# Optimization experiments

Hardware: AMD Instinct MI355X
Metric: run time of the kernel (lower is better)

The kernel has to match this reference:

```python
import jax, jax.numpy as jnp
import numpy as np


def conv2d(x, w, bias, stride=1, pad=0, groups=1):
    out = jax.lax.conv_general_dilated(
        x, w, (stride, stride), [(pad, pad), (pad, pad)],
        dimension_numbers=("NCHW", "OIHW", "NCHW"), feature_group_count=groups)
    return out + bias[None, :, None, None]


PATCHSIZE = [(4, 4), (8, 8)]
NEG = jnp.float32(-1e9)


def setup_inputs() -> dict:
    key = jax.random.key(0)
    ks = jax.random.split(key, 24)
    d = 128
    s = 0.05
    inp = {
        "x": jax.random.normal(ks[0], (16, d, 64, 64), jnp.float32),
        "m": jax.random.uniform(ks[1], (16, 1, 64, 64), jnp.float32),
        "depth_map": jax.random.normal(ks[2], (16, 1, 256, 256), jnp.float32),
        "wq": jax.random.normal(ks[3], (d, d, 1, 1), jnp.float32) * s,
        "bq": jax.random.normal(ks[4], (d,), jnp.float32) * s,
        "wk": jax.random.normal(ks[5], (d, d, 1, 1), jnp.float32) * s,
        "bk": jax.random.normal(ks[6], (d,), jnp.float32) * s,
        "wv": jax.random.normal(ks[7], (d, d, 1, 1), jnp.float32) * s,
        "bv": jax.random.normal(ks[8], (d,), jnp.float32) * s,
        "wvle": jax.random.normal(ks[9], (d, 1, 3, 3), jnp.float32) * s,  # depthwise
        "bvle": jax.random.normal(ks[10], (d,), jnp.float32) * s,
        "wd1": jax.random.normal(ks[11], (d, 1, 3, 3), jnp.float32) * s,
        "bd1": jax.random.normal(ks[12], (d,), jnp.float32) * s,
        "wd2": jax.random.normal(ks[13], (1, d, 3, 3), jnp.float32) * s,
        "bd2": jax.random.normal(ks[14], (1,), jnp.float32) * s,
        "wo": jax.random.normal(ks[15], (d, d, 3, 3), jnp.float32) * s,
        "bo": jax.random.normal(ks[16], (d,), jnp.float32) * s,
        "b": 2,
        "c": 128,
    }
    return inp


def _forward(x, m, depth_map, wq, bq, wk, bk, wv, bv, wvle, bvle,
             wd1, bd1, wd2, bd2, wo, bo, b, c):
    bt, _, h, w = x.shape
    t = bt // b
    d_k = c // len(PATCHSIZE)

    q_all = conv2d(x, wq, bq)
    k_all = conv2d(x, wk, bk)
    v_all = conv2d(x, wv, bv) + conv2d(x, wvle, bvle, pad=1, groups=c)
    d1 = jax.nn.relu(conv2d(depth_map, wd1, bd1, stride=2, pad=1))
    _depth = jax.nn.relu(conv2d(d1, wd2, bd2, stride=2, pad=1))  # (bt,1,h,w)

    outs = []
    for i, (width, height) in enumerate(PATCHSIZE):
        out_w, out_h = w // width, h // height
        L = t * out_h * out_w

        def patch(z, ch):
            # (b*t, ch, h, w) -> (b, L, ch*height*width)
            z = z.reshape(b, t, ch, out_h, height, out_w, width)
            return z.transpose(0, 1, 3, 5, 2, 4, 6).reshape(b, L, ch * height * width)

        mask = jnp.mean(patch(m, 1), -1) > 0.5            # (b, L) per-key mask
        dsort = jnp.sort(patch(_depth, 1), -1)            # (b, L, height*width)
        hw = height * width
        dmin, dmed, dmax = dsort[..., 0], dsort[..., (hw - 1) // 2], dsort[..., -1]

        q = patch(q_all[:, i * d_k:(i + 1) * d_k], d_k)
        k_ = patch(k_all[:, i * d_k:(i + 1) * d_k], d_k)
        v = patch(v_all[:, i * d_k:(i + 1) * d_k], d_k)

        scale = 1.0 / jnp.sqrt(jnp.float32(q.shape[-1]))
        s = jnp.einsum("bqd,bkd->bqk", q, k_) * scale     # shared QK^T

        def head(dbias):
            ss = s * jax.nn.sigmoid(dbias)[:, None, :]
            ss = jnp.where(mask[:, None, :], NEG, ss)
            return jnp.einsum("bqk,bkd->bqd", jax.nn.softmax(ss, -1), v)

        y = (head(dmed) + head(dmax) + head(dmin)) / 3.0
        y = y.reshape(b, t, out_h, out_w, d_k, height, width)
        y = y.transpose(0, 1, 4, 2, 5, 3, 6).reshape(bt, d_k, h, w)
        outs.append(y)

    out = jnp.concatenate(outs, 1)
    out = conv2d(out, wo, bo, pad=1)
    out = jnp.where(out >= 0, out, 0.2 * out)  # LeakyReLU(0.2)
    return out


def reference(x, m, depth_map, wq, bq, wk, bk, wv, bv, wvle, bvle,
              wd1, bd1, wd2, bd2, wo, bo, b, c):
    out = _forward(x, m, depth_map, wq, bq, wk, bk, wv, bv, wvle, bvle,
                   wd1, bd1, wd2, bd2, wo, bo, b, c)
    return (out, depth_map)
```

## Files before the change

kernel.cpp:

```cpp
#include <hip/hip_runtime.h>
#include <cmath>

typedef unsigned short u16;
typedef __attribute__((ext_vector_type(8))) __bf16 bf16x8;
typedef __attribute__((ext_vector_type(4))) float f32x4;

constexpr int Bb = 2, Tt = 8, Dc = 128, PIX = 4096;

__device__ inline u16 f2bf(float f) {
    unsigned u = __builtin_bit_cast(unsigned, f);
    u += 0x7fffu + ((u >> 16) & 1u);
    return (u16)(u >> 16);
}
__device__ inline float bf2f(u16 h) {
    unsigned u = ((unsigned)h) << 16;
    return __builtin_bit_cast(float, u);
}

#define GLOAD16(gp, lp) __builtin_amdgcn_global_load_lds( \
    (const __attribute__((address_space(1))) void*)(const void*)(gp), \
    (__attribute__((address_space(3))) void*)(void*)(lp), 16, 0, 0)

__device__ inline void mfma_chunk(const u16* lAs, const u16* lBs, int wave, int lane,
                                  f32x4 (&acc)[4][4])
{
    const int wm = (wave >> 1) * 64, wn = (wave & 1) * 64;
    const int fr = lane & 15;
    const int q4 = lane >> 4;
    const int sw = (q4 ^ ((fr >> 1) & 3)) * 8;
    bf16x8 av[4], bv[4];
#pragma unroll
    for (int i = 0; i < 4; ++i) av[i] = *(const bf16x8*)&lAs[(wm + i * 16 + fr) * 32 + sw];
#pragma unroll
    for (int j = 0; j < 4; ++j) bv[j] = *(const bf16x8*)&lBs[(wn + j * 16 + fr) * 32 + sw];
#pragma unroll
    for (int i = 0; i < 4; ++i)
#pragma unroll
        for (int j = 0; j < 4; ++j)
            acc[i][j] = __builtin_amdgcn_mfma_f32_16x16x32_bf16(av[i], bv[j], acc[i][j], 0, 0, 0);
}

__device__ inline void mfma_nt(const u16* A, int ldkA, const u16* B, int ldkB,
                               int kChunks, int wave, int lane,
                               u16* lAs, u16* lBs, f32x4 (&acc)[4][4])
{
    const int r = lane >> 2;
    const int kq8 = ((lane & 3) ^ ((r >> 1) & 3)) * 8;
    const u16* ga0 = A + (size_t)(wave * 32 + r) * ldkA + kq8;
    const u16* ga1 = ga0 + (size_t)16 * ldkA;
    const u16* gb0 = B + (size_t)(wave * 32 + r) * ldkB + kq8;
    const u16* gb1 = gb0 + (size_t)16 * ldkB;
    for (int kb = 0; kb < kChunks; kb += 2) {
        __syncthreads();
        GLOAD16(ga0 + kb * 32, lAs + wave * 1024);
        GLOAD16(ga1 + kb * 32, lAs + wave * 1024 + 512);
        GLOAD16(gb0 + kb * 32, lBs + wave * 1024);
        GLOAD16(gb1 + kb * 32, lBs + wave * 1024 + 512);
        GLOAD16(ga0 + (kb + 1) * 32, lAs + 4096 + wave * 1024);
        GLOAD16(ga1 + (kb + 1) * 32, lAs + 4096 + wave * 1024 + 512);
        GLOAD16(gb0 + (kb + 1) * 32, lBs + 4096 + wave * 1024);
        GLOAD16(gb1 + (kb + 1) * 32, lBs + 4096 + wave * 1024 + 512);
        __syncthreads();
        mfma_chunk(lAs, lBs, wave, lane, acc);
        mfma_chunk(lAs + 4096, lBs + 4096, wave, lane, acc);
    }
}

__global__ void k_prep(const float* __restrict__ wq, const float* __restrict__ wk,
                       const float* __restrict__ wv, const float* __restrict__ wo,
                       u16* __restrict__ Wqkv, u16* __restrict__ WoT)
{
    int idx = blockIdx.x * 256 + threadIdx.x;
    if (idx < 49152) {
        const float* w = idx < 16384 ? wq : (idx < 32768 ? wk : wv);
        Wqkv[idx] = f2bf(w[idx & 16383]);
    }
    int j = idx - 49152;
    if (j >= 0 && j < 147456) {
        int tap = j / 16384, rem = j % 16384;
        WoT[j] = f2bf(wo[(size_t)rem * 9 + tap]);
    }
}

__global__ __launch_bounds__(256) void k_xt(const float* __restrict__ x, u16* __restrict__ Xt)
{
    __shared__ float ls[128 * 65];
    const int n = blockIdx.y, pix0 = blockIdx.x * 64;
#pragma unroll
    for (int rep = 0; rep < 32; ++rep) {
        int idx = rep * 256 + threadIdx.x;
        int cin = idx >> 6, p = idx & 63;
        ls[cin * 65 + p] = x[((size_t)n * Dc + cin) * PIX + pix0 + p];
    }
    __syncthreads();
#pragma unroll
    for (int rep = 0; rep < 32; ++rep) {
        int idx = rep * 256 + threadIdx.x;
        int p = idx >> 7, cin = idx & 127;
        Xt[((size_t)n * PIX + pix0 + p) * Dc + cin] = f2bf(ls[cin * 65 + p]);
    }
}

__global__ __launch_bounds__(256) void k_qkv_mfma(const u16* __restrict__ Wqkv,
                                                  const u16* __restrict__ Xt,
                                                  const float* __restrict__ bq,
                                                  const float* __restrict__ bk,
                                                  const float* __restrict__ bv,
                                                  u16* __restrict__ Qp0, u16* __restrict__ Kp0,
                                                  u16* __restrict__ Qp1, u16* __restrict__ Kp1,
                                                  u16* __restrict__ v_bf)
{
    __shared__ u16 lAs[8192], lBs[8192];
    const int tid = threadIdx.x, wave = tid >> 6, lane = tid & 63;
    const int mt = blockIdx.y, n = blockIdx.z, px0 = blockIdx.x * 128;
    f32x4 acc[4][4];
#pragma unroll
    for (int i = 0; i < 4; ++i)
#pragma unroll
        for (int j = 0; j < 4; ++j) acc[i][j] = (f32x4){0.f, 0.f, 0.f, 0.f};
    mfma_nt(Wqkv + (size_t)mt * 128 * 128, 128,
            Xt + ((size_t)n * PIX + px0) * 128, 128, 4, wave, lane, lAs, lBs, acc);
    const int wm = (wave >> 1) * 64, wn = (wave & 1) * 64;
    const int rb = (lane >> 4) * 4, cb = lane & 15;
    const int bi = n >> 3, ti = n & 7;
    if (mt < 2) {
        const float* bp = (mt == 0) ? bq : bk;
        u16* d0 = (mt == 0) ? Qp0 : Kp0;
        u16* d1 = (mt == 0) ? Qp1 : Kp1;
#pragma unroll
        for (int i = 0; i < 4; ++i)
#pragma unroll
            for (int reg = 0; reg < 4; ++reg) {
                int c = wm + i * 16 + rb + reg;
                float bias = bp[c];
#pragma unroll
                for (int j = 0; j < 4; ++j) {
                    int pix = px0 + wn + j * 16 + cb;
                    int y = pix >> 6, x = pix & 63;
                    u16 val = f2bf(acc[i][j][reg] + bias);
                    if (c < 64) {
                        int l = ti * 256 + (y >> 2) * 16 + (x >> 2);
                        int f = c * 16 + (y & 3) * 4 + (x & 3);
                        d0[((size_t)bi * 2048 + l) * 1024 + f] = val;
                    } else {
                        int l = ti * 64 + (y >> 3) * 8 + (x >> 3);
                        int f = (c - 64) * 64 + (y & 7) * 8 + (x & 7);
                        d1[((size_t)bi * 512 + l) * 4096 + f] = val;
                    }
                }
            }
    } else {
#pragma unroll
        for (int i = 0; i < 4; ++i)
#pragma unroll
            for (int reg = 0; reg < 4; ++reg) {
                int c = wm + i * 16 + rb + reg;
                float bias = bv[c];
#pragma unroll
                for (int j = 0; j < 4; ++j) {
                    int pix = px0 + wn + j * 16 + cb;
                    v_bf[((size_t)n * Dc + c) * PIX + pix] = f2bf(acc[i][j][reg] + bias);
                }
            }
    }
}

__global__ __launch_bounds__(256) void k_vdw(const float* __restrict__ X,
                                             const float* __restrict__ wvle,
                                             const float* __restrict__ bvle,
                                             u16* __restrict__ v_bf)
{
    __shared__ float ls[4096];
    const int c = blockIdx.x, n = blockIdx.y;
    const int tid = threadIdx.x;
    const float* xp = X + ((size_t)n * Dc + c) * PIX;
#pragma unroll
    for (int r = 0; r < 4; ++r)
        *(float4*)&ls[r * 1024 + tid * 4] = *(const float4*)&xp[r * 1024 + tid * 4];
    __syncthreads();
    float w[9];
#pragma unroll
    for (int t = 0; t < 9; ++t) w[t] = wvle[c * 9 + t];
    const float bias = bvle[c];
    const int x = tid & 63, y0 = (tid >> 6) * 16;
    const bool xl = (x > 0), xr = (x < 63);
    u16* vp = v_bf + ((size_t)n * Dc + c) * PIX;
#pragma unroll
    for (int r = 0; r < 16; ++r) {
        int y = y0 + r;
        float s = bias;
#pragma unroll
        for (int ky = 0; ky < 3; ++ky) {
            int yy = y + ky - 1;
            if (yy < 0 || yy > 63) continue;
            const float* row = &ls[yy * 64];
            float m  = row[x];
            float lv = xl ? row[x - 1] : 0.f;
            float rv = xr ? row[x + 1] : 0.f;
            s += w[ky * 3 + 0] * lv + w[ky * 3 + 1] * m + w[ky * 3 + 2] * rv;
        }
        int idx = y * 64 + x;
        vp[idx] = f2bf(bf2f(vp[idx]) + s);
    }
}

__global__ __launch_bounds__(256) void k_d1(const float* __restrict__ dm,
                                            const float* __restrict__ wd1,
                                            const float* __restrict__ bd1,
                                            u16* __restrict__ d1b)
{
    __shared__ float ls[17 * 132];
    const int n = blockIdx.y;
    const int yt = blockIdx.x >> 1, xh = blockIdx.x & 1;
    const int Y0 = yt * 8;
    const int tid = threadIdx.x;
    const float* dmp = dm + (size_t)n * 65536;
    for (int idx = tid; idx < 17 * 132; idx += 256) {
        int row = idx / 132, cl = idx % 132;
        int gr = 2 * Y0 - 1 + row;
        int gc = 128 * xh - 1 + cl;
        float v = 0.f;
        if (gr >= 0 && gr < 256 && gc >= 0 && gc < 256 && cl < 129) v = dmp[gr * 256 + gc];
        ls[idx] = v;
    }
    __syncthreads();
    const int Xl = tid & 63;
    const int Yl0 = tid >> 6;
    float in0[9], in1[9];
#pragma unroll
    for (int jy = 0; jy < 3; ++jy)
#pragma unroll
        for (int jx = 0; jx < 3; ++jx) {
            in0[jy * 3 + jx] = ls[(2 * Yl0 + jy) * 132 + 2 * Xl + jx];
            in1[jy * 3 + jx] = ls[(2 * (Yl0 + 4) + jy) * 132 + 2 * Xl + jx];
        }
    const int X = 64 * xh + Xl;
    u16* outbase = d1b + (size_t)n * Dc * 16384 + (size_t)Y0 * 128 + X;
    for (int c = 0; c < 128; ++c) {
        const float* w1 = wd1 + c * 9;
        float a0 = bd1[c], a1 = a0;
#pragma unroll
        for (int t = 0; t < 9; ++t) { a0 += w1[t] * in0[t]; a1 += w1[t] * in1[t]; }
        u16* ob = outbase + (size_t)c * 16384;
        ob[(size_t)Yl0 * 128]       = f2bf(fmaxf(a0, 0.f));
        ob[(size_t)(Yl0 + 4) * 128] = f2bf(fmaxf(a1, 0.f));
    }
}

__global__ __launch_bounds__(256) void k_d2p(const u16* __restrict__ d1b,
                                             const float* __restrict__ wd2,
                                             float* __restrict__ part)
{
    __shared__ u16 ls[33 * 136];
    const int yt = blockIdx.x, n = blockIdx.y, cg = blockIdx.z;
    const int tid = threadIdx.x;
    const int y0 = yt * 16;
    if (tid < 33) ls[tid * 136 + 7] = 0;
    const int x = tid & 63;
    const int yl0 = (tid >> 6) * 4;
    float acc[4] = {0.f, 0.f, 0.f, 0.f};
    for (int c = 0; c < 16; ++c) {
        const u16* src = d1b + ((size_t)n * Dc + cg * 16 + c) * 16384;
        __syncthreads();
        for (int idx = tid; idx < 33 * 16; idx += 256) {
            int row = idx >> 4, s = idx & 15;
            int gr = 2 * y0 - 1 + row;
            uint4 v = make_uint4(0, 0, 0, 0);
            if (gr >= 0 && gr < 128) v = *(const uint4*)(src + gr * 128 + s * 8);
            *(uint4*)&ls[row * 136 + 8 + s * 8] = v;
        }
        __syncthreads();
        const float* w2 = wd2 + (cg * 16 + c) * 9;
        float w[9];
#pragma unroll
        for (int t = 0; t < 9; ++t) w[t] = w2[t];
#pragma unroll
        for (int r = 0; r < 4; ++r) {
            int yl = yl0 + r;
#pragma unroll
            for (int ky = 0; ky < 3; ++ky) {
                const u16* rp = &ls[(2 * yl + ky) * 136 + 2 * x + 7];
                float v0 = bf2f(rp[0]);
                unsigned pr = *(const unsigned*)(rp + 1);
                float v1 = bf2f((u16)(pr & 0xffffu));
                float v2 = bf2f((u16)(pr >> 16));
                acc[r] += w[ky * 3 + 0] * v0 + w[ky * 3 + 1] * v1 + w[ky * 3 + 2] * v2;
            }
        }
    }
    float* pp = part + ((size_t)cg * 16 + n) * PIX;
#pragma unroll
    for (int r = 0; r < 4; ++r)
        pp[(y0 + yl0 + r) * 64 + x] = acc[r];
}

__global__ void k_dfin(const float* __restrict__ part, const float* __restrict__ bd2,
                       float* __restrict__ dep)
{
    int idx = blockIdx.x * 256 + threadIdx.x;
    float s = bd2[0];
#pragma unroll
    for (int cg = 0; cg < 8; ++cg) s += part[(size_t)cg * 65536 + idx];
    dep[idx] = fmaxf(s, 0.f);
}

template<int PS>
__global__ __launch_bounds__(256) void k_stats2(const float* __restrict__ mI,
                                                const float* __restrict__ dep,
                                                float* __restrict__ maskf,
                                                float* __restrict__ smed,
                                                float* __restrict__ smaxA,
                                                float* __restrict__ sminA,
                                                int outn, int L)
{
    constexpr int HW = PS * PS;
    constexpr int TPB = 256 / HW;
    const int tok = blockIdx.x * TPB + threadIdx.x / HW;
    const int el  = threadIdx.x % HW;
    if (tok >= Bb * L) return;
    const int bi = tok / L, l = tok % L;
    const int ti = l / (outn * outn); const int rem = l % (outn * outn);
    const int oh = rem / outn, ow = rem % outn;
    const int n = bi * Tt + ti;
    const int py = el / PS, px = el % PS;
    const size_t off = (size_t)n * PIX + (size_t)(oh * PS + py) * 64 + ow * PS + px;
    const float mv = mI[off];
    const float dv = dep[off];
    float msum = mv, vmin = dv, vmax = dv;
#pragma unroll
    for (int o = HW / 2; o > 0; o >>= 1) {
        msum += __shfl_xor(msum, o);
        vmin = fminf(vmin, __shfl_xor(vmin, o));
        vmax = fmaxf(vmax, __shfl_xor(vmax, o));
    }
    const int gbase = (threadIdx.x & 63) & ~(HW - 1);
    int cl = 0, ce = 0;
#pragma unroll
    for (int b2 = 0; b2 < HW; ++b2) {
        float vb = __shfl(dv, gbase + b2);
        cl += (vb < dv);
        ce += (vb == dv);
    }
    constexpr int kk = (HW - 1) / 2;
    if (el == 0) {
        maskf[tok] = (msum / (float)HW > 0.5f) ? 1.f : 0.f;
        smaxA[tok] = 1.f / (1.f + __expf(-vmax));
        sminA[tok] = 1.f / (1.f + __expf(-vmin));
    }
    if (cl <= kk && kk < cl + ce)
        smed[tok] = 1.f / (1.f + __expf(-dv));
}

__global__ void k_patchT(const u16* __restrict__ v_bf, u16* __restrict__ Vt,
                         int ps, int outn, int L, int F, int cbase)
{
    size_t idx = (size_t)blockIdx.x * 256 + threadIdx.x;
    size_t total = (size_t)Bb * F * L / 4;
    if (idx >= total) return;
    int l0 = (int)((idx * 4) % L);
    size_t t2 = (idx * 4) / L;
    int f = (int)(t2 % F);
    int bi = (int)(t2 / F);
    int hw = ps * ps;
    int c = cbase + f / hw, r = f % hw;
    int py = r / ps, px = r % ps;
    int ti = l0 / (outn * outn); int rem = l0 % (outn * outn);
    int oh = rem / outn, ow0 = rem % outn;
    size_t base = ((size_t)(bi * Tt + ti) * Dc + c) * PIX + (oh * ps + py) * 64 + px;
    u16 out4[4];
#pragma unroll
    for (int e = 0; e < 4; ++e) out4[e] = v_bf[base + (size_t)(ow0 + e) * ps];
    *(uint2*)&Vt[((size_t)bi * F + f) * L + l0] = *(uint2*)out4;
}

__global__ __launch_bounds__(256) void k_qkT_mfma(const u16* __restrict__ Qp,
                                                  const u16* __restrict__ Kp,
                                                  u16* __restrict__ S,
                                                  int L, int F, int ksplit, float scale)
{
    __shared__ u16 lAs[8192], lBs[8192];
    const int tid = threadIdx.x, wave = tid >> 6, lane = tid & 63;
    const int bi = blockIdx.z / ksplit, ks = blockIdx.z % ksplit;
    const int kf = F / ksplit;
    f32x4 acc[4][4];
#pragma unroll
    for (int i = 0; i < 4; ++i)
#pragma unroll
        for (int j = 0; j < 4; ++j) acc[i][j] = (f32x4){0.f, 0.f, 0.f, 0.f};
    mfma_nt(Qp + (size_t)bi * L * F + (size_t)blockIdx.y * 128 * F + (size_t)ks * kf, F,
            Kp + (size_t)bi * L * F + (size_t)blockIdx.x * 128 * F + (size_t)ks * kf, F,
            kf / 32, wave, lane, lAs, lBs, acc);
    const int wm = (wave >> 1) * 64, wn = (wave & 1) * 64;
    const int rb = (lane >> 4) * 4, cb = lane & 15;
    u16* Cp = S + ((size_t)ks * Bb + bi) * L * L;
#pragma unroll
    for (int i = 0; i < 4; ++i)
#pragma unroll
        for (int reg = 0; reg < 4; ++reg) {
            int gm = blockIdx.y * 128 + wm + i * 16 + rb + reg;
#pragma unroll
            for (int j = 0; j < 4; ++j) {
                int gn = blockIdx.x * 128 + wn + j * 16 + cb;
                Cp[(size_t)gm * L + gn] = f2bf(acc[i][j][reg] * scale);
            }
        }
}

__device__ inline float blockMax(float v, float* sh) {
#pragma unroll
    for (int o = 32; o > 0; o >>= 1) v = fmaxf(v, __shfl_down(v, o));
    __syncthreads();
    if ((threadIdx.x & 63) == 0) sh[threadIdx.x >> 6] = v;
    __syncthreads();
    return fmaxf(fmaxf(sh[0], sh[1]), fmaxf(sh[2], sh[3]));
}
__device__ inline float blockSum(float v, float* sh) {
#pragma unroll
    for (int o = 32; o > 0; o >>= 1) v += __shfl_down(v, o);
    __syncthreads();
    if ((threadIdx.x & 63) == 0) sh[threadIdx.x >> 6] = v;
    __syncthreads();
    return sh[0] + sh[1] + sh[2] + sh[3];
}

template<int NPAIR, int NSPLIT>
__global__ __launch_bounds__(256) void k_softmax(const u16* __restrict__ S,
                                                 u16* __restrict__ Pb,
                                                 const float* __restrict__ maskf,
                                                 const float* __restrict__ smed,
                                                 const float* __restrict__ smaxA,
                                                 const float* __restrict__ sminA,
                                                 int L)
{
    __shared__ float sred[4];
    const int bi = blockIdx.y, q = blockIdx.x;
    const size_t pstr = (size_t)Bb * L * L;
    const u16* row = S + (size_t)bi * L * L + (size_t)q * L;
    u16* prow = Pb + (size_t)bi * L * L + (size_t)q * L;
    const float* mk  = maskf + bi * L;
    const float* s0p = smed  + bi * L;
    const float* s1p = smaxA + bi * L;
    const float* s2p = sminA + bi * L;
    const int tid = threadIdx.x;
    float a0[2 * NPAIR], a1[2 * NPAIR], a2[2 * NPAIR];
    float m0 = -3.4e38f, m1 = -3.4e38f, m2 = -3.4e38f;
#pragma unroll
    for (int e = 0; e < NPAIR; ++e) {
        int k = e * 512 + tid * 2;
        unsigned u = *(const unsigned*)&row[k];
        float sva = bf2f((u16)(u & 0xffffu));
        float svb = bf2f((u16)(u >> 16));
#pragma unroll
        for (int s2 = 1; s2 < NSPLIT; ++s2) {
            unsigned w = *(const unsigned*)&row[(size_t)s2 * pstr + k];
            sva += bf2f((u16)(w & 0xffffu));
            svb += bf2f((u16)(w >> 16));
        }
        float2 mv  = *(const float2*)&mk[k];
        float2 p0  = *(const float2*)&s0p[k];
        float2 p1  = *(const float2*)&s1p[k];
        float2 p2  = *(const float2*)&s2p[k];
        bool ma = mv.x > 0.5f, mb = mv.y > 0.5f;
        float v0a = ma ? -1e9f : sva * p0.x, v0b = mb ? -1e9f : svb * p0.y;
        float v1a = ma ? -1e9f : sva * p1.x, v1b = mb ? -1e9f : svb * p1.y;
        float v2a = ma ? -1e9f : sva * p2.x, v2b = mb ? -1e9f : svb * p2.y;
        a0[2 * e] = v0a; a0[2 * e + 1] = v0b;
        a1[2 * e] = v1a; a1[2 * e + 1] = v1b;
        a2[2 * e] = v2a; a2[2 * e + 1] = v2b;
        m0 = fmaxf(m0, fmaxf(v0a, v0b));
        m1 = fmaxf(m1, fmaxf(v1a, v1b));
        m2 = fmaxf(m2, fmaxf(v2a, v2b));
    }
    m0 = blockMax(m0, sred); m1 = blockMax(m1, sred); m2 = blockMax(m2, sred);
    float l0 = 0.f, l1 = 0.f, l2 = 0.f;
#pragma unroll
    for (int e = 0; e < 2 * NPAIR; ++e) {
        a0[e] = __expf(a0[e] - m0); l0 += a0[e];
        a1[e] = __expf(a1[e] - m1); l1 += a1[e];
        a2[e] = __expf(a2[e] - m2); l2 += a2[e];
    }
    l0 = blockSum(l0, sred); l1 = blockSum(l1, sred); l2 = blockSum(l2, sred);
    float c0 = 1.f / (3.f * l0), c1 = 1.f / (3.f * l1), c2 = 1.f / (3.f * l2);
#pragma unroll
    for (int e = 0; e < NPAIR; ++e) {
        int k = e * 512 + tid * 2;
        u16 oa = f2bf(a0[2 * e] * c0 + a1[2 * e] * c1 + a2[2 * e] * c2);
        u16 ob = f2bf(a0[2 * e + 1] * c0 + a1[2 * e + 1] * c1 + a2[2 * e + 1] * c2);
        unsigned pk = (unsigned)oa | ((unsigned)ob << 16);
        *(unsigned*)&prow[k] = pk;
    }
}

__global__ __launch_bounds__(256) void k_pv_mfma(const u16* __restrict__ Pb,
                                                 const u16* __restrict__ Vt,
                                                 u16* __restrict__ Yp,
                                                 int L, int F, int ksplit)
{
    __shared__ u16 lAs[8192], lBs[8192];
    const int tid = threadIdx.x, wave = tid >> 6, lane = tid & 63;
    const int bi = blockIdx.z / ksplit, ks = blockIdx.z % ksplit;
    const int kf = L / ksplit;
    f32x4 acc[4][4];
#pragma unroll
    for (int i = 0; i < 4; ++i)
#pragma unroll
        for (int j = 0; j < 4; ++j) acc[i][j] = (f32x4){0.f, 0.f, 0.f, 0.f};
    mfma_nt(Pb + (size_t)bi * L * L + (size_t)blockIdx.y * 128 * L + (size_t)ks * kf, L,
            Vt + (size_t)bi * F * L + (size_t)blockIdx.x * 128 * L + (size_t)ks * kf, L,
            kf / 32, wave, lane, lAs, lBs, acc);
    const int wm = (wave >> 1) * 64, wn = (wave & 1) * 64;
    const int rb = (lane >> 4) * 4, cb = lane & 15;
    u16* Cp = Yp + ((size_t)(ks * Bb + bi) * L) * F;
#pragma unroll
    for (int i = 0; i < 4; ++i)
#pragma unroll
        for (int reg = 0; reg < 4; ++reg) {
            int gm = blockIdx.y * 128 + wm + i * 16 + rb + reg;
#pragma unroll
            for (int j = 0; j < 4; ++j) {
                int gn = blockIdx.x * 128 + wn + j * 16 + cb;
                Cp[(size_t)gm * F + gn] = f2bf(acc[i][j][reg]);
            }
        }
}

template<int NSPLIT>
__global__ void k_unpatch(const u16* __restrict__ Yp, u16* __restrict__ catbT,
                          int ps, int outn, int L, int F, int cbase)
{
    size_t idx = (size_t)blockIdx.x * 256 + threadIdx.x;
    size_t total = (size_t)Bb * L * F / 4;
    if (idx >= total) return;
    const size_t pstr = (size_t)Bb * L * F;
    int f0 = (int)((idx * 4) % F);
    size_t t2 = (idx * 4) / F;
    int l = (int)(t2 % L);
    int bi = (int)(t2 / L);
    size_t off = ((size_t)bi * L + l) * F + f0;
    float s[4] = {0.f, 0.f, 0.f, 0.f};
#pragma unroll
    for (int sp = 0; sp < NSPLIT; ++sp) {
        uint2 u = *(const uint2*)&Yp[(size_t)sp * pstr + off];
        s[0] += bf2f((u16)(u.x & 0xffffu));
        s[1] += bf2f((u16)(u.x >> 16));
        s[2] += bf2f((u16)(u.y & 0xffffu));
        s[3] += bf2f((u16)(u.y >> 16));
    }
    int hw = ps * ps;
    int c = cbase + f0 / hw, r0 = f0 % hw;
    int ti = l / (outn * outn); int rem = l % (outn * outn);
    int oh = rem / outn, ow = rem % outn;
    int n = bi * Tt + ti;
    int py = r0 / ps, px = r0 % ps;
    size_t base = ((size_t)n * PIX + (size_t)(oh * ps + py) * 64 + ow * ps + px) * Dc + c;
#pragma unroll
    for (int e = 0; e < 4; ++e)
        catbT[base + (size_t)e * Dc] = f2bf(s[e]);
}

__global__ __launch_bounds__(256) void k_conv_mfma(const u16* __restrict__ catbT,
                                                   const u16* __restrict__ WoT,
                                                   const u16* __restrict__ zp,
                                                   u16* __restrict__ Cpart)
{
    __shared__ u16 lAs[8192], lBs[8192];
    const int tid = threadIdx.x, wave = tid >> 6, lane = tid & 63;
    const int pix0 = blockIdx.x * 128;
    const int sp = blockIdx.y;
    const int r = lane >> 2;
    const int kq8 = ((lane & 3) ^ ((r >> 1) & 3)) * 8;
    int yb[2], xb[2], nn[2];
#pragma unroll
    for (int s = 0; s < 2; ++s) {
        int pg = pix0 + wave * 32 + r + s * 16;
        nn[s] = pg >> 12; yb[s] = (pg >> 6) & 63; xb[s] = pg & 63;
    }
    const u16* gb_base = WoT + (size_t)(wave * 32 + r) * 128 + kq8;
    f32x4 acc[4][4];
#pragma unroll
    for (int i = 0; i < 4; ++i)
#pragma unroll
        for (int j = 0; j < 4; ++j) acc[i][j] = (f32x4){0.f, 0.f, 0.f, 0.f};
    for (int tp = 0; tp < 9; ++tp) {
        const int t0 = sp * 18 + tp * 2;
        __syncthreads();
#pragma unroll
        for (int h = 0; h < 2; ++h) {
            const int t = t0 + h;
            const int tap = t >> 2, kc = t & 3;
            const int dy = tap / 3 - 1, dx = tap % 3 - 1;
            const u16* ga[2];
#pragma unroll
            for (int s = 0; s < 2; ++s) {
                int y = yb[s] + dy, xx = xb[s] + dx;
                bool ok = ((unsigned)y < 64u) && ((unsigned)xx < 64u);
                ga[s] = ok ? catbT + (((size_t)(nn[s] << 12) + y * 64 + xx) << 7) + kq8 + kc * 32 : zp;
            }
            const u16* gb = gb_base + tap * 16384 + kc * 32;
            GLOAD16(ga[0], lAs + h * 4096 + wave * 1024);
            GLOAD16(ga[1], lAs + h * 4096 + wave * 1024 + 512);
            GLOAD16(gb, lBs + h * 4096 + wave * 1024);
            GLOAD16(gb + 2048, lBs + h * 4096 + wave * 1024 + 512);
        }
        __syncthreads();
        mfma_chunk(lAs, lBs, wave, lane, acc);
        mfma_chunk(lAs + 4096, lBs + 4096, wave, lane, acc);
    }
    const int wm = (wave >> 1) * 64, wn = (wave & 1) * 64;
    const int rb = (lane >> 4) * 4, cb = lane & 15;
    u16* Cp = Cpart + (size_t)sp * 8388608;
#pragma unroll
    for (int i = 0; i < 4; ++i)
#pragma unroll
        for (int reg = 0; reg < 4; ++reg) {
            int gm = pix0 + wm + i * 16 + rb + reg;
#pragma unroll
            for (int j = 0; j < 4; ++j) {
                int gn = wn + j * 16 + cb;
                Cp[(size_t)gm * 128 + gn] = f2bf(acc[i][j][reg]);
            }
        }
}

__global__ __launch_bounds__(256) void k_cfin(const u16* __restrict__ Cpart,
                                              const float* __restrict__ bo,
                                              float* __restrict__ outp)
{
    const int pg0 = blockIdx.x * 64;
    const int lane = threadIdx.x & 63, wv = threadIdx.x >> 6;
    const int pix = pg0 + lane;
    const int n = pix >> 12, p = pix & 4095;
    const u16* r0 = Cpart + (size_t)pix * 128 + wv * 32;
    const u16* r1 = r0 + 8388608;
#pragma unroll
    for (int c4 = 0; c4 < 8; ++c4) {
        uint2 a = *(const uint2*)(r0 + c4 * 4);
        uint2 b = *(const uint2*)(r1 + c4 * 4);
        float s[4];
        s[0] = bf2f((u16)(a.x & 0xffffu)) + bf2f((u16)(b.x & 0xffffu));
        s[1] = bf2f((u16)(a.x >> 16))     + bf2f((u16)(b.x >> 16));
        s[2] = bf2f((u16)(a.y & 0xffffu)) + bf2f((u16)(b.y & 0xffffu));
        s[3] = bf2f((u16)(a.y >> 16))     + bf2f((u16)(b.y >> 16));
#pragma unroll
        for (int e = 0; e < 4; ++e) {
            int cout = wv * 32 + c4 * 4 + e;
            float v = s[e] + bo[cout];
            v = (v >= 0.f) ? v : 0.2f * v;
            outp[((size_t)n * Dc + cout) * PIX + p] = v;
        }
    }
}

extern "C" void kernel_launch(void* const* d_in, const int* in_sizes, int n_in,
                              void* d_out, int out_size, void* d_ws, size_t ws_size,
                              hipStream_t stream)
{
    (void)in_sizes; (void)n_in; (void)out_size; (void)ws_size;
    const float* x    = (const float*)d_in[0];
    const float* mI   = (const float*)d_in[1];
    const float* dmap = (const float*)d_in[2];
    const float* wq   = (const float*)d_in[3];
    const float* bq   = (const float*)d_in[4];
    const float* wk   = (const float*)d_in[5];
    const float* bk   = (const float*)d_in[6];
    const float* wv   = (const float*)d_in[7];
    const float* bv   = (const float*)d_in[8];
    const float* wvle = (const float*)d_in[9];
    const float* bvle = (const float*)d_in[10];
    const float* wd1  = (const float*)d_in[11];
    const float* bd1  = (const float*)d_in[12];
    const float* wd2  = (const float*)d_in[13];
    const float* bd2  = (const float*)d_in[14];
    const float* wo   = (const float*)d_in[15];
    const float* bo   = (const float*)d_in[16];

    char* w8 = (char*)d_ws;
    u16*   v_bf  = (u16*)(w8);
    u16*   Xt    = (u16*)(w8 + 0x1000000);
    u16*   catbT = (u16*)(w8 + 0x2000000);
    u16*   Qp0   = (u16*)(w8 + 0x3000000);
    u16*   Kp0   = (u16*)(w8 + 0x3800000);
    u16*   Qp1   = (u16*)(w8 + 0x4000000);
    u16*   Kp1   = (u16*)(w8 + 0x4800000);
    u16*   Vt    = (u16*)(w8 + 0x5000000);
    u16*   Sb    = (u16*)(w8 + 0x5800000);
    u16*   Pb    = (u16*)(w8 + 0x7800000);
    u16*   Yp    = (u16*)(w8 + 0x8800000);
    u16*   Cpart = (u16*)(w8 + 0x5800000);
    u16*   d1b   = (u16*)(w8 + 0x3000000);
    float* dep   = (float*)(w8 + 0xA800000);
    float* maskf = (float*)(w8 + 0xA840000);
    float* smed  = (float*)(w8 + 0xA844000);
    float* smaxA = (float*)(w8 + 0xA848000);
    float* sminA = (float*)(w8 + 0xA84C000);
    u16*   Wqkv  = (u16*)(w8 + 0xA850000);
    u16*   WoT   = (u16*)(w8 + 0xA868000);
    u16*   zp    = (u16*)(w8 + 0xA8B0000);
    float* part  = (float*)(w8 + 0xA8C0000);
    float* outp  = (float*)d_out;

    hipMemcpyAsync(outp + 8388608, dmap, (size_t)16 * 65536 * sizeof(float),
                   hipMemcpyDeviceToDevice, stream);
    hipMemsetAsync(zp, 0, 256, stream);

    dim3 blk(256);
    k_d1<<<dim3(32, 16), blk, 0, stream>>>(dmap, wd1, bd1, d1b);
    k_d2p<<<dim3(4, 16, 8), blk, 0, stream>>>(d1b, wd2, part);
    k_dfin<<<dim3(256), blk, 0, stream>>>(part, bd2, dep);

    k_prep<<<dim3(768), blk, 0, stream>>>(wq, wk, wv, wo, Wqkv, WoT);
    k_xt<<<dim3(64, 16), blk, 0, stream>>>(x, Xt);
    k_qkv_mfma<<<dim3(32, 3, 16), blk, 0, stream>>>(Wqkv, Xt, bq, bk, bv,
                                                    Qp0, Kp0, Qp1, Kp1, v_bf);
    k_vdw<<<dim3(128, 16), blk, 0, stream>>>(x, wvle, bvle, v_bf);

    for (int i = 0; i < 2; ++i) {
        const int ps = (i == 0) ? 4 : 8;
        const int outn = 64 / ps;
        const int L = Tt * outn * outn;
        const int F = 64 * ps * ps;
        const int cbase = i * 64;
        const float scale = 1.0f / sqrtf((float)F);
        const int ksplit  = (i == 0) ? 2 : 16;
        const int pvsplit = 4;
        const u16* Qp = (i == 0) ? Qp0 : Qp1;
        const u16* Kp = (i == 0) ? Kp0 : Kp1;

        if (i == 0) k_stats2<4><<<dim3(Bb * L * 16 / 256), blk, 0, stream>>>(mI, dep, maskf, smed, smaxA, sminA, outn, L);
        else        k_stats2<8><<<dim3(Bb * L * 64 / 256), blk, 0, stream>>>(mI, dep, maskf, smed, smaxA, sminA, outn, L);

        const int pgrid = (int)(((size_t)Bb * L * F / 4 + 255) / 256);
        k_patchT<<<dim3(pgrid), blk, 0, stream>>>(v_bf, Vt, ps, outn, L, F, cbase);

        k_qkT_mfma<<<dim3(L / 128, L / 128, Bb * ksplit), blk, 0, stream>>>(Qp, Kp, Sb, L, F, ksplit, scale);

        if (i == 0) k_softmax<4, 2><<<dim3(L, Bb), blk, 0, stream>>>(Sb, Pb, maskf, smed, smaxA, sminA, L);
        else        k_softmax<1, 16><<<dim3(L, Bb), blk, 0, stream>>>(Sb, Pb, maskf, smed, smaxA, sminA, L);

        k_pv_mfma<<<dim3(F / 128, L / 128, Bb * pvsplit), blk, 0, stream>>>(Pb, Vt, Yp, L, F, pvsplit);
        k_unpatch<4><<<dim3(pgrid), blk, 0, stream>>>(Yp, catbT, ps, outn, L, F, cbase);
    }

    k_conv_mfma<<<dim3(512, 2), blk, 0, stream>>>(catbT, WoT, zp, Cpart);
    k_cfin<<<dim3(1024), blk, 0, stream>>>(Cpart, bo, outp);
}
```

Measured before the change: 436.2 us.

## Fuse depth conv stages into one kernel recomputing d1 in registers

Replaces the two-kernel depth path (stride-2 depthwise conv writing a bf16 intermediate, then a reducing stride-2 conv) with a single kernel that loads a 7x8 window of the depth map per output pixel and recomputes the needed d1 values on the fly. This removes the write and re-read of the large per-channel intermediate buffer and one launch. In exchange it recomputes each d1 value several times and keeps it in fp32 rather than bf16. The channel split for partial sums drops from 8 to 4 groups.

Result: faster. 417.6 us (-4.3%).

```diff
diff --git a/kernel.cpp b/kernel.cpp
--- a/kernel.cpp
+++ b/kernel.cpp
@@ -204,94 +204,56 @@
     }
 }
 
-__global__ __launch_bounds__(256) void k_d1(const float* __restrict__ dm,
-                                            const float* __restrict__ wd1,
-                                            const float* __restrict__ bd1,
-                                            u16* __restrict__ d1b)
-{
-    __shared__ float ls[17 * 132];
-    const int n = blockIdx.y;
-    const int yt = blockIdx.x >> 1, xh = blockIdx.x & 1;
-    const int Y0 = yt * 8;
-    const int tid = threadIdx.x;
+__global__ __launch_bounds__(256) void k_depth(const float* __restrict__ dm,
+                                               const float* __restrict__ wd1,
+                                               const float* __restrict__ bd1,
+                                               const float* __restrict__ wd2,
+                                               float* __restrict__ part)
+{
+    const int tile = blockIdx.x, n = blockIdx.y, cs = blockIdx.z;
+    const int ty = threadIdx.x >> 4, tx = threadIdx.x & 15;
+    const int y = (tile >> 2) * 16 + ty;
+    const int x = (tile & 3) * 16 + tx;
     const float* dmp = dm + (size_t)n * 65536;
-    for (int idx = tid; idx < 17 * 132; idx += 256) {
-        int row = idx / 132, cl = idx % 132;
-        int gr = 2 * Y0 - 1 + row;
-        int gc = 128 * xh - 1 + cl;
-        float v = 0.f;
-        if (gr >= 0 && gr < 256 && gc >= 0 && gc < 256 && cl < 129) v = dmp[gr * 256 + gc];
-        ls[idx] = v;
-    }
-    __syncthreads();
-    const int Xl = tid & 63;
-    const int Yl0 = tid >> 6;
-    float in0[9], in1[9];
-#pragma unroll
-    for (int jy = 0; jy < 3; ++jy)
-#pragma unroll
-        for (int jx = 0; jx < 3; ++jx) {
-            in0[jy * 3 + jx] = ls[(2 * Yl0 + jy) * 132 + 2 * Xl + jx];
-            in1[jy * 3 + jx] = ls[(2 * (Yl0 + 4) + jy) * 132 + 2 * Xl + jx];
-        }
-    const int X = 64 * xh + Xl;
-    u16* outbase = d1b + (size_t)n * Dc * 16384 + (size_t)Y0 * 128 + X;
-    for (int c = 0; c < 128; ++c) {
+    float f[7][8];
+    const int gc0 = 4 * x - 4;
+#pragma unroll
+    for (int r = 0; r < 7; ++r) {
+        const int gr = 4 * y - 3 + r;
+        const float* rp = dmp + gr * 256 + gc0;
+        const bool rok = (gr >= 0);
+        float4 va = (rok && x > 0) ? *(const float4*)rp
+                                   : make_float4(0.f, 0.f, 0.f, 0.f);
+        float4 vb = rok ? *(const float4*)(rp + 4)
+                        : make_float4(0.f, 0.f, 0.f, 0.f);
+        f[r][0] = va.x; f[r][1] = va.y; f[r][2] = va.z; f[r][3] = va.w;
+        f[r][4] = vb.x; f[r][5] = vb.y; f[r][6] = vb.z; f[r][7] = vb.w;
+    }
+    const bool vy = (y > 0), vx = (x > 0);
+    float acc = 0.f;
+    const int c0 = cs * 32;
+#pragma unroll 2
+    for (int cc = 0; cc < 32; ++cc) {
+        const int c = c0 + cc;
         const float* w1 = wd1 + c * 9;
-        float a0 = bd1[c], a1 = a0;
-#pragma unroll
-        for (int t = 0; t < 9; ++t) { a0 += w1[t] * in0[t]; a1 += w1[t] * in1[t]; }
-        u16* ob = outbase + (size_t)c * 16384;
-        ob[(size_t)Yl0 * 128]       = f2bf(fmaxf(a0, 0.f));
-        ob[(size_t)(Yl0 + 4) * 128] = f2bf(fmaxf(a1, 0.f));
-    }
-}
-
-__global__ __launch_bounds__(256) void k_d2p(const u16* __restrict__ d1b,
-                                             const float* __restrict__ wd2,
-                                             float* __restrict__ part)
-{
-    __shared__ u16 ls[33 * 136];
-    const int yt = blockIdx.x, n = blockIdx.y, cg = blockIdx.z;
-    const int tid = threadIdx.x;
-    const int y0 = yt * 16;
-    if (tid < 33) ls[tid * 136 + 7] = 0;
-    const int x = tid & 63;
-    const int yl0 = (tid >> 6) * 4;
-    float acc[4] = {0.f, 0.f, 0.f, 0.f};
-    for (int c = 0; c < 16; ++c) {
-        const u16* src = d1b + ((size_t)n * Dc + cg * 16 + c) * 16384;
-        __syncthreads();
-        for (int idx = tid; idx < 33 * 16; idx += 256) {
-            int row = idx >> 4, s = idx & 15;
-            int gr = 2 * y0 - 1 + row;
-            uint4 v = make_uint4(0, 0, 0, 0);
-            if (gr >= 0 && gr < 128) v = *(const uint4*)(src + gr * 128 + s * 8);
-            *(uint4*)&ls[row * 136 + 8 + s * 8] = v;
-        }
-        __syncthreads();
-        const float* w2 = wd2 + (cg * 16 + c) * 9;
-        float w[9];
-#pragma unroll
-        for (int t = 0; t < 9; ++t) w[t] = w2[t];
-#pragma unroll
-        for (int r = 0; r < 4; ++r) {
-            int yl = yl0 + r;
-#pragma unroll
-            for (int ky = 0; ky < 3; ++ky) {
-                const u16* rp = &ls[(2 * yl + ky) * 136 + 2 * x + 7];
-                float v0 = bf2f(rp[0]);
-                unsigned pr = *(const unsigned*)(rp + 1);
-                float v1 = bf2f((u16)(pr & 0xffffu));
-                float v2 = bf2f((u16)(pr >> 16));
-                acc[r] += w[ky * 3 + 0] * v0 + w[ky * 3 + 1] * v1 + w[ky * 3 + 2] * v2;
+        const float* w2 = wd2 + c * 9;
+        const float b1 = bd1[c];
+#pragma unroll
+        for (int jy = 0; jy < 3; ++jy)
+#pragma unroll
+            for (int jx = 0; jx < 3; ++jx) {
+                float s = b1;
+#pragma unroll
+                for (int ky = 0; ky < 3; ++ky)
+#pragma unroll
+                    for (int kx = 0; kx < 3; ++kx)
+                        s += w1[ky * 3 + kx] * f[2 * jy + ky][2 * jx + kx + 1];
+                s = fmaxf(s, 0.f);
+                const bool ok = (jy > 0 || vy) && (jx > 0 || vx);
+                acc += w2[jy * 3 + jx] * (ok ? s : 0.f);
             }
-        }
-    }
-    float* pp = part + ((size_t)cg * 16 + n) * PIX;
-#pragma unroll
-    for (int r = 0; r < 4; ++r)
-        pp[(y0 + yl0 + r) * 64 + x] = acc[r];
+    }
+    part[((size_t)cs * 16 + n) * PIX + y * 64 + x] = acc;
 }
 
 __global__ void k_dfin(const float* __restrict__ part, const float* __restrict__ bd2,
@@ -300,7 +262,7 @@
     int idx = blockIdx.x * 256 + threadIdx.x;
     float s = bd2[0];
 #pragma unroll
-    for (int cg = 0; cg < 8; ++cg) s += part[(size_t)cg * 65536 + idx];
+    for (int cg = 0; cg < 4; ++cg) s += part[(size_t)cg * 65536 + idx];
     dep[idx] = fmaxf(s, 0.f);
 }
 
@@ -687,7 +649,6 @@
     u16*   Pb    = (u16*)(w8 + 0x7800000);
     u16*   Yp    = (u16*)(w8 + 0x8800000);
     u16*   Cpart = (u16*)(w8 + 0x5800000);
-    u16*   d1b   = (u16*)(w8 + 0x3000000);
     float* dep   = (float*)(w8 + 0xA800000);
     float* maskf = (float*)(w8 + 0xA840000);
     float* smed  = (float*)(w8 + 0xA844000);
@@ -704,8 +665,7 @@
     hipMemsetAsync(zp, 0, 256, stream);
 
     dim3 blk(256);
-    k_d1<<<dim3(32, 16), blk, 0, stream>>>(dmap, wd1, bd1, d1b);
-    k_d2p<<<dim3(4, 16, 8), blk, 0, stream>>>(d1b, wd2, part);
+    k_depth<<<dim3(16, 16, 4), blk, 0, stream>>>(dmap, wd1, bd1, wd2, part);
     k_dfin<<<dim3(256), blk, 0, stream>>>(part, bd2, dep);
 
     k_prep<<<dim3(768), blk, 0, stream>>>(wq, wk, wv, wo, Wqkv, WoT);
```
